# Performance work log

Measured on AMD Instinct MI355X. Metric: run time of the kernel, lower is better.

The kernel has to match this reference:

```python
import jax, jax.numpy as jnp
import numpy as np

K_MASK = -2.3819763e+38
ROPE_THETA = 1000000
MROPE_SECTION = (24, 20, 20)
NORM_EPS = 1e-6


def rms_norm(x, w, eps=NORM_EPS):
    dtype = x.dtype
    x32 = x.astype(jnp.float32)
    rms_inv = jax.lax.rsqrt(jnp.mean(x32 * x32, axis=-1, keepdims=True) + eps)
    return w * (x32 * rms_inv).astype(dtype)


def apply_rope(inputs, positions, head_dim, rope_theta=ROPE_THETA, mrope_section=MROPE_SECTION):
    # positions: [3, B, T] (temporal, height, width); inputs: [B, T, heads, head_dim]
    fraction = 2 * jnp.arange(0, head_dim // 2, dtype=jnp.float32) / head_dim
    timescale = rope_theta ** fraction  # [head_dim//2]
    sinusoid = positions[:, :, :, None].astype(jnp.float32) / timescale  # [3,B,T,hd/2]
    freq = sinusoid[0]
    h_idx = jnp.arange(1, mrope_section[1] * 3, 3)
    w_idx = jnp.arange(2, mrope_section[2] * 3, 3)
    freq = freq.at[..., h_idx].set(sinusoid[1][..., h_idx])
    freq = freq.at[..., w_idx].set(sinusoid[2][..., w_idx])
    freq = freq[:, :, None, :]  # [B,T,1,hd/2]
    sin, cos = jnp.sin(freq), jnp.cos(freq)
    first, second = jnp.split(inputs, 2, axis=-1)
    out = jnp.concatenate([first * cos - second * sin, second * cos + first * sin], axis=-1)
    return out.astype(inputs.dtype)


def setup_inputs() -> dict:
    key = jax.random.key(0)
    ks = jax.random.split(key, 6)
    B, T, D, N, K, H = 2, 1024, 2560, 32, 8, 128
    x = jax.random.normal(ks[0], (B, T, D), dtype=jnp.float32)
    positions = jnp.broadcast_to(jnp.arange(T, dtype=jnp.int32), (3, B, T))
    attn_mask = jnp.tril(jnp.ones((T, T), dtype=bool))[None].repeat(B, axis=0)  # causal [B,T,T]
    wq = jax.random.normal(ks[1], (D, N, H), dtype=jnp.float32) * 0.02
    wk = jax.random.normal(ks[2], (D, K, H), dtype=jnp.float32) * 0.02
    wv = jax.random.normal(ks[3], (D, K, H), dtype=jnp.float32) * 0.02
    wo = jax.random.normal(ks[4], (N, H, D), dtype=jnp.float32) * 0.02
    q_norm_w = jnp.ones((H,), dtype=jnp.float32)
    k_norm_w = jnp.ones((H,), dtype=jnp.float32)
    return {"x": x, "positions": positions, "attn_mask": attn_mask, "wq": wq,
            "wk": wk, "wv": wv, "wo": wo, "q_norm_w": q_norm_w, "k_norm_w": k_norm_w}


def reference(x, positions, attn_mask, wq, wk, wv, wo, q_norm_w, k_norm_w):
    head_dim = wo.shape[1]
    scale = head_dim ** -0.5
    q = rms_norm(jnp.einsum('btd,dnh->btnh', x, wq), q_norm_w)
    k = rms_norm(jnp.einsum('bsd,dkh->bskh', x, wk), k_norm_w)
    v = jnp.einsum('bsd,dkh->bskh', x, wv)
    q = apply_rope(q, positions, head_dim)
    k = apply_rope(k, positions, head_dim)
    b, t, qh, d = q.shape
    _, s, kh, _ = k.shape
    q = q.reshape((b, t, kh, qh // kh, d))  # GQA grouping
    attn = jnp.einsum('bthgd,bshd->bhgts', q, k) * scale
    attn = attn.reshape((b, qh, t, s))
    attn = jnp.where(attn_mask[:, None, :, :], attn, K_MASK)
    attn = jax.nn.softmax(attn.astype(jnp.float32), axis=-1).astype(k.dtype)
    attn = attn.reshape((b, kh, qh // kh, t, s))
    qkv = jnp.einsum('bhgts,bshd->bthgd', attn, v).reshape((b, t, qh, d))
    return jnp.einsum('btnh,nhd->btd', qkv, wo)
```

## Files before the change

kernel.cpp:

```cpp
#include <hip/hip_runtime.h>
#include <hip/hip_bf16.h>

typedef __attribute__((ext_vector_type(8))) __bf16 bf8_t;
typedef __attribute__((ext_vector_type(4))) float f32x4;
typedef __attribute__((ext_vector_type(16))) float f32x16;

#define GLOAD16(gptr, lptr)                                                              \
  __builtin_amdgcn_global_load_lds((const __attribute__((address_space(1))) void*)(gptr), \
                                   (__attribute__((address_space(3))) void*)(lptr), 16, 0, 0)

__device__ __forceinline__ unsigned short f2bf(float f) {
  union { float f; unsigned u; } v; v.f = f;
  return (unsigned short)((v.u + 0x7fffu + ((v.u >> 16) & 1u)) >> 16);
}

__device__ __forceinline__ float bf2f(unsigned short u) {
  union { unsigned u; float f; } v; v.u = ((unsigned)u) << 16;
  return v.f;
}

__device__ __forceinline__ unsigned cvtpk_bf16(float a, float b) {
  unsigned r;
  asm("v_cvt_pk_bf16_f32 %0, %1, %2" : "=v"(r) : "v"(a), "v"(b));
  return r;
}

__global__ void cast_bf16(const float* __restrict__ in, unsigned short* __restrict__ out, int n4) {
  int i = blockIdx.x * blockDim.x + threadIdx.x;
  if (i >= n4) return;
  float4 v = ((const float4*)in)[i];
  ushort4 o;
  o.x = f2bf(v.x); o.y = f2bf(v.y); o.z = f2bf(v.z); o.w = f2bf(v.w);
  ((ushort4*)out)[i] = o;
}

__global__ void tcast(const float* __restrict__ in, unsigned short* __restrict__ out,
                      int R, int C, int ld, int rowOff) {
  __shared__ float tile[32][33];
  int c0 = blockIdx.x * 32, r0 = blockIdx.y * 32;
  int tx = threadIdx.x, ty = threadIdx.y;
#pragma unroll
  for (int i = 0; i < 4; ++i)
    tile[ty + 8 * i][tx] = in[(size_t)(r0 + ty + 8 * i) * C + c0 + tx];
  __syncthreads();
#pragma unroll
  for (int i = 0; i < 4; ++i)
    out[(size_t)(rowOff + c0 + ty + 8 * i) * ld + r0 + tx] = f2bf(tile[tx][ty + 8 * i]);
}

__global__ __launch_bounds__(512, 2) void gemm256(
    const unsigned short* __restrict__ A,
    const unsigned short* __restrict__ Bt,
    float* __restrict__ C0, float* __restrict__ C1,
    unsigned short* __restrict__ Cb,
    int N, int ldk, int Kslice, int nTileN) {
  __shared__ unsigned short SM[4][2][8192];
  int ks = blockIdx.y;
  int kbase = ks * Kslice;
  int nwg = gridDim.x;
  int bidx = blockIdx.x;
  int wg = ((bidx & 7) * (nwg >> 3)) + (bidx >> 3);
  int bm = wg / nTileN, bn = wg % nTileN;
  int m0 = bm << 8, n0 = bn << 8;
  int tid = threadIdx.x, lane = tid & 63, w = tid >> 6;
  int wm = w >> 2, wn = w & 3;
  int lrow = lane & 15, lch = lane >> 4;
  int srow = tid >> 2;
  int scol = ((tid & 3) ^ ((srow >> 1) & 3)) << 3;
  int nt = Kslice >> 5;

  f32x4 acc[8][4] = {};

  auto stage = [&](int t) {
    int buf = t & 3;
    int k0 = kbase + (t << 5);
    const unsigned short* Ag = A + (size_t)(m0 + srow) * ldk + k0 + scol;
    const unsigned short* Bg = Bt + (size_t)(n0 + srow) * ldk + k0 + scol;
    unsigned short* Al = &SM[buf][0][w << 9];
    unsigned short* Bl = &SM[buf][1][w << 9];
    GLOAD16(Ag, Al);
    GLOAD16(Ag + (size_t)128 * ldk, Al + 4096);
    GLOAD16(Bg, Bl);
    GLOAD16(Bg + (size_t)128 * ldk, Bl + 4096);
  };

  stage(0);
  stage(1);
  stage(2);
  for (int t = 0; t < nt; ++t) {
    if (t + 2 < nt)      asm volatile("s_waitcnt vmcnt(8)" ::: "memory");
    else if (t + 1 < nt) asm volatile("s_waitcnt vmcnt(4)" ::: "memory");
    else                 asm volatile("s_waitcnt vmcnt(0)" ::: "memory");
    asm volatile("s_barrier" ::: "memory");
    if (t + 3 < nt) stage(t + 3);
    int buf = t & 3;
    const unsigned short* As = &SM[buf][0][0];
    const unsigned short* Bs = &SM[buf][1][0];
    bf8_t a[8], b[4];
#pragma unroll
    for (int mi = 0; mi < 8; ++mi) {
      int ar = (wm << 7) + (mi << 4) + lrow;
      a[mi] = *(const bf8_t*)(As + ar * 32 + ((lch ^ ((ar >> 1) & 3)) << 3));
    }
#pragma unroll
    for (int ni = 0; ni < 4; ++ni) {
      int br = (wn << 6) + (ni << 4) + lrow;
      b[ni] = *(const bf8_t*)(Bs + br * 32 + ((lch ^ ((br >> 1) & 3)) << 3));
    }
    __builtin_amdgcn_s_setprio(1);
#pragma unroll
    for (int mi = 0; mi < 8; ++mi)
#pragma unroll
      for (int ni = 0; ni < 4; ++ni)
        acc[mi][ni] = __builtin_amdgcn_mfma_f32_16x16x32_bf16(a[mi], b[ni], acc[mi][ni], 0, 0, 0);
    __builtin_amdgcn_s_setprio(0);
  }
  int r0 = m0 + (wm << 7) + (lch << 2);
  int c0 = n0 + (wn << 6) + lrow;
  if (Cb) {
#pragma unroll
    for (int mi = 0; mi < 8; ++mi)
#pragma unroll
      for (int ni = 0; ni < 4; ++ni)
#pragma unroll
        for (int r = 0; r < 4; ++r)
          Cb[(size_t)(r0 + (mi << 4) + r) * N + c0 + (ni << 4)] = f2bf(acc[mi][ni][r]);
  } else {
    float* __restrict__ C = ks ? C1 : C0;
#pragma unroll
    for (int mi = 0; mi < 8; ++mi)
#pragma unroll
      for (int ni = 0; ni < 4; ++ni)
#pragma unroll
        for (int r = 0; r < 4; ++r)
          C[(size_t)(r0 + (mi << 4) + r) * N + c0 + (ni << 4)] = acc[mi][ni][r];
  }
}

__global__ void reduce_add(const float4* __restrict__ a, const float4* __restrict__ b,
                           float4* __restrict__ o, int n4) {
  int i = blockIdx.x * blockDim.x + threadIdx.x;
  if (i >= n4) return;
  float4 x = a[i], y = b[i];
  o[i] = make_float4(x.x + y.x, x.y + y.y, x.z + y.z, x.w + y.w);
}

__global__ __launch_bounds__(128) void normrope(
    const unsigned short* __restrict__ qkv, const int* __restrict__ positions,
    const float* __restrict__ qw, const float* __restrict__ kw,
    unsigned short* __restrict__ qb, unsigned short* __restrict__ kb,
    unsigned short* __restrict__ vt) {
  int blk = blockIdx.x;
  int hh = blk % 48, bt = blk / 48;
  int b = bt >> 10, t = bt & 1023;
  int tid = threadIdx.x;
  int colbase = (hh < 32) ? (hh << 7) : ((hh < 40) ? (4096 + ((hh - 32) << 7)) : (5120 + ((hh - 40) << 7)));
  float val = bf2f(qkv[(size_t)bt * 6144 + colbase + tid]);
  if (hh >= 40) {
    vt[((size_t)((b * 8 + hh - 40) * 128 + tid)) * 1024 + t] = f2bf(val);
    return;
  }
  __shared__ float red[2];
  __shared__ float xs[128];
  float ss = val * val;
#pragma unroll
  for (int m = 32; m >= 1; m >>= 1) ss += __shfl_xor(ss, m);
  if ((tid & 63) == 0) red[tid >> 6] = ss;
  __syncthreads();
  float rinv = rsqrtf((red[0] + red[1]) * (1.0f / 128.0f) + 1e-6f);
  float wgt = (hh < 32) ? qw[tid] : kw[tid];
  float xn = val * rinv * wgt;
  xs[tid] = xn;
  __syncthreads();
  float other = xs[tid ^ 64];
  int pos = positions[b * 1024 + t];
  int j = tid & 63;
  float ang = (float)pos * exp2f(-(float)j * 0.31143075889569027f);
  float sv = sinf(ang), cv = cosf(ang);
  float outv = (tid < 64) ? (xn * cv - other * sv) : (xn * cv + other * sv);
  if (hh >= 32) outv *= 0.12751744f;
  unsigned short o = f2bf(outv);
  if (hh < 32) qb[((size_t)((b * 32 + hh) * 1024 + t)) * 128 + tid] = o;
  else kb[((size_t)((b * 8 + hh - 32) * 1024 + t)) * 128 + tid] = o;
}

__global__ __launch_bounds__(256, 2) void attn(
    const unsigned short* __restrict__ qb,
    const unsigned short* __restrict__ kb,
    const unsigned short* __restrict__ vt,
    unsigned short* __restrict__ ob) {
  __shared__ unsigned short Kl[2][64 * 128];
  __shared__ unsigned short Vl[2][128 * 64];
  int bx = blockIdx.x, hq = blockIdx.y, b = blockIdx.z;
  int qt = (bx < 4) ? (7 - bx) : (bx - 4);
  int kvh = hq >> 2;
  int tid = threadIdx.x, lane = tid & 63, w = tid >> 6;
  int qlane = lane & 31, h = lane >> 5;
  int q0 = (qt << 7) + (w << 5);
  int qg = q0 + qlane;
  const unsigned short* kbase = kb + ((size_t)(b * 8 + kvh) << 17);
  const unsigned short* vbase = vt + ((size_t)(b * 8 + kvh) << 17);

  const unsigned short* qptr = qb + ((size_t)((b * 32 + hq) * 1024 + qg) << 7) + (h << 3);
  bf8_t qf[8];
#pragma unroll
  for (int ds = 0; ds < 8; ++ds) qf[ds] = *(const bf8_t*)(qptr + ds * 16);

  f32x16 o[4] = {};
  float mrun = -3.0e38f, lrun = 0.f;
  int last_st = (q0 + 31) >> 6;
  int nsteps = 2 * qt + 2;

  auto stage = [&](int st, int buf) {
    int s0 = st << 6;
    unsigned short* kd = &Kl[buf][0];
    unsigned short* vd = &Vl[buf][0];
#pragma unroll
    for (int i = 0; i < 4; ++i) {
      int cid = i * 256 + tid;
      int kr = cid >> 4, ksl = cid & 15;
      GLOAD16(kbase + (size_t)(s0 + kr) * 128 + ((ksl ^ (kr & 15)) << 3), kd + cid * 8);
      int vr = cid >> 3, vsl = cid & 7;
      GLOAD16(vbase + (size_t)vr * 1024 + s0 + ((vsl ^ (vr & 7)) << 3), vd + cid * 8);
    }
  };

  stage(0, 0);
  for (int st = 0; st < nsteps; ++st) {
    __syncthreads();
    if (st + 1 < nsteps) stage(st + 1, (st + 1) & 1);
    if (st <= last_st) {
      const char* Kb = (const char*)&Kl[st & 1][0];
      const char* Vb = (const char*)&Vl[st & 1][0];
      f32x16 s0v = {}, s1v = {};
      __builtin_amdgcn_s_setprio(1);
#pragma unroll
      for (int ds = 0; ds < 8; ++ds) {
        int c = ds * 2 + h;
        int r0 = qlane, r1 = 32 + qlane;
        bf8_t k0 = *(const bf8_t*)(Kb + r0 * 256 + ((c ^ (r0 & 15)) << 4));
        bf8_t k1 = *(const bf8_t*)(Kb + r1 * 256 + ((c ^ (r1 & 15)) << 4));
        s0v = __builtin_amdgcn_mfma_f32_32x32x16_bf16(k0, qf[ds], s0v, 0, 0, 0);
        s1v = __builtin_amdgcn_mfma_f32_32x32x16_bf16(k1, qf[ds], s1v, 0, 0, 0);
      }
      __builtin_amdgcn_s_setprio(0);
      bool dm = (st == last_st);
      int kg0 = st << 6;
      float mt = -3.0e38f;
#pragma unroll
      for (int e = 0; e < 16; ++e) {
        int kl = (e & 3) + 8 * (e >> 2) + 4 * h;
        if (dm) {
          if (kg0 + kl > qg) s0v[e] = -3.0e38f;
          if (kg0 + 32 + kl > qg) s1v[e] = -3.0e38f;
        }
        mt = fmaxf(mt, fmaxf(s0v[e], s1v[e]));
      }
      mt = fmaxf(mt, __shfl_xor(mt, 32));
      if (!__all(mt - mrun <= 8.0f)) {
        float mnew = fmaxf(mrun, mt);
        float alpha = exp2f(mrun - mnew);
        lrun *= alpha;
#pragma unroll
        for (int db = 0; db < 4; ++db)
#pragma unroll
          for (int e = 0; e < 16; ++e) o[db][e] *= alpha;
        mrun = mnew;
      }
      float ls = 0.f;
#pragma unroll
      for (int e = 0; e < 16; ++e) {
        s0v[e] = exp2f(s0v[e] - mrun);
        s1v[e] = exp2f(s1v[e] - mrun);
        ls += s0v[e] + s1v[e];
      }
      ls += __shfl_xor(ls, 32);
      lrun += ls;
      bf8_t pf[4];
#pragma unroll
      for (int s = 0; s < 4; ++s) {
        unsigned w00, w01, w10, w11;
        {
          const int B0 = 4 * ((2 * s) & 3);
          if ((2 * s) >> 2) { w00 = cvtpk_bf16(s1v[B0], s1v[B0 + 1]); w01 = cvtpk_bf16(s1v[B0 + 2], s1v[B0 + 3]); }
          else              { w00 = cvtpk_bf16(s0v[B0], s0v[B0 + 1]); w01 = cvtpk_bf16(s0v[B0 + 2], s0v[B0 + 3]); }
        }
        {
          const int B1 = 4 * ((2 * s + 1) & 3);
          if ((2 * s + 1) >> 2) { w10 = cvtpk_bf16(s1v[B1], s1v[B1 + 1]); w11 = cvtpk_bf16(s1v[B1 + 2], s1v[B1 + 3]); }
          else                  { w10 = cvtpk_bf16(s0v[B1], s0v[B1 + 1]); w11 = cvtpk_bf16(s0v[B1 + 2], s0v[B1 + 3]); }
        }
        unsigned sa = h ? w00 : w10, sb = h ? w01 : w11;
        unsigned ra = __shfl_xor(sa, 32), rb = __shfl_xor(sb, 32);
        unsigned ka = h ? w10 : w00, kb2 = h ? w11 : w01;
        unsigned f0 = h ? ra : ka, f1 = h ? rb : kb2;
        unsigned f2 = h ? ka : ra, f3 = h ? kb2 : rb;
        uint4 fv = make_uint4(f0, f1, f2, f3);
        pf[s] = *(bf8_t*)&fv;
      }
      __builtin_amdgcn_s_setprio(1);
#pragma unroll
      for (int db = 0; db < 4; ++db) {
        int vr = (db << 5) + qlane;
#pragma unroll
        for (int s = 0; s < 4; ++s) {
          int c = (s << 1) + h;
          bf8_t vf = *(const bf8_t*)(Vb + vr * 128 + ((c ^ (vr & 7)) << 4));
          o[db] = __builtin_amdgcn_mfma_f32_32x32x16_bf16(vf, pf[s], o[db], 0, 0, 0);
        }
      }
      __builtin_amdgcn_s_setprio(0);
    }
  }

  __syncthreads();
  unsigned short* tb = &Kl[0][0] + (w << 12);
  float inv = 1.0f / lrun;
#pragma unroll
  for (int db = 0; db < 4; ++db)
#pragma unroll
    for (int rq = 0; rq < 4; ++rq) {
      int d0 = (db << 5) + (rq << 3) + (h << 2);
      unsigned lo = ((unsigned)f2bf(o[db][rq * 4 + 1] * inv) << 16) | f2bf(o[db][rq * 4 + 0] * inv);
      unsigned hi = ((unsigned)f2bf(o[db][rq * 4 + 3] * inv) << 16) | f2bf(o[db][rq * 4 + 2] * inv);
      *(uint2*)(tb + qlane * 128 + (d0 ^ ((qlane & 15) << 3))) = make_uint2(lo, hi);
    }
  int rr = lane >> 1, dh = (lane & 1) << 6;
  size_t orow = ((size_t)(b * 1024 + q0 + rr) << 12) + (hq << 7);
#pragma unroll
  for (int i = 0; i < 8; ++i) {
    int d8 = dh + i * 8;
    uint4 vv = *(const uint4*)(tb + rr * 128 + (d8 ^ ((rr & 15) << 3)));
    *(uint4*)(&ob[orow + d8]) = vv;
  }
}

extern "C" void kernel_launch(void* const* d_in, const int* in_sizes, int n_in,
                              void* d_out, int out_size, void* d_ws, size_t ws_size,
                              hipStream_t stream) {
  const float* x = (const float*)d_in[0];
  const int* positions = (const int*)d_in[1];
  const float* wq = (const float*)d_in[3];
  const float* wk = (const float*)d_in[4];
  const float* wv = (const float*)d_in[5];
  const float* wo = (const float*)d_in[6];
  const float* qnw = (const float*)d_in[7];
  const float* knw = (const float*)d_in[8];
  float* out = (float*)d_out;

  char* ws = (char*)d_ws;
  unsigned short* x_bf  = (unsigned short*)(ws);
  unsigned short* wqkvT = (unsigned short*)(ws + 10485760);
  unsigned short* woT   = (unsigned short*)(ws + 41943040);
  unsigned short* qkvb  = (unsigned short*)(ws + 62914560);
  float*          p0    = (float*)(ws + 62914560);
  float*          p1    = (float*)(ws + 83886080);
  unsigned short* q_bf  = (unsigned short*)(ws + 113246208);
  unsigned short* k_bf  = (unsigned short*)(ws + 130023424);
  unsigned short* vt_bf = (unsigned short*)(ws + 134217728);
  unsigned short* a_bf  = (unsigned short*)(ws + 138412032);

  cast_bf16<<<5120, 256, 0, stream>>>(x, x_bf, 2048 * 2560 / 4);
  tcast<<<dim3(128, 80), dim3(32, 8), 0, stream>>>(wq, wqkvT, 2560, 4096, 2560, 0);
  tcast<<<dim3(32, 80), dim3(32, 8), 0, stream>>>(wk, wqkvT, 2560, 1024, 2560, 4096);
  tcast<<<dim3(32, 80), dim3(32, 8), 0, stream>>>(wv, wqkvT, 2560, 1024, 2560, 5120);
  tcast<<<dim3(80, 128), dim3(32, 8), 0, stream>>>(wo, woT, 4096, 2560, 4096, 0);
  gemm256<<<dim3(8 * 24, 1), 512, 0, stream>>>(x_bf, wqkvT, nullptr, nullptr, qkvb,
                                               6144, 2560, 2560, 24);
  normrope<<<2048 * 48, 128, 0, stream>>>(qkvb, positions, qnw, knw, q_bf, k_bf, vt_bf);
  attn<<<dim3(8, 32, 2), 256, 0, stream>>>(q_bf, k_bf, vt_bf, a_bf);
  gemm256<<<dim3(8 * 10, 2), 512, 0, stream>>>(a_bf, woT, p0, p1, nullptr, 2560, 4096, 2048, 10);
  reduce_add<<<5120, 256, 0, stream>>>((const float4*)p0, (const float4*)p1, (float4*)out,
                                       2048 * 2560 / 4);
}
```

Baseline: 282.9 us.

## Vectorize weight transpose-cast, load V directly to registers, three-way split-K output GEMM

Replaces the transpose-cast kernel with a wider variant that reads float4 and writes 16-byte bf16 rows, cutting per-thread memory instructions. The attention kernel no longer stages V through LDS and instead loads V fragments straight from global memory into registers, halving LDS use and async copy traffic. The output projection GEMM moves from a two-way to a three-way split-K with an uneven last slice, and the reduction now sums three partials. This adds more blocks for occupancy but increases partial-buffer traffic, and the direct V loads may expose global latency.

New measurement: 288.9 us. +2.1%, slower.

```diff
diff --git a/kernel.cpp b/kernel.cpp
--- a/kernel.cpp
+++ b/kernel.cpp
@@ -34,29 +34,48 @@
   ((ushort4*)out)[i] = o;
 }
 
-__global__ void tcast(const float* __restrict__ in, unsigned short* __restrict__ out,
-                      int R, int C, int ld, int rowOff) {
-  __shared__ float tile[32][33];
-  int c0 = blockIdx.x * 32, r0 = blockIdx.y * 32;
-  int tx = threadIdx.x, ty = threadIdx.y;
+__global__ __launch_bounds__(256) void tcast4(const float* __restrict__ in,
+                                              unsigned short* __restrict__ out,
+                                              int C, int ld, int rowOff) {
+  __shared__ float tile[128][40];
+  int c0 = blockIdx.x * 128, r0 = blockIdx.y * 32;
+  int tid = threadIdx.x;
+  int tx = tid & 31, ty = tid >> 5;
+  float4 v[4];
 #pragma unroll
   for (int i = 0; i < 4; ++i)
-    tile[ty + 8 * i][tx] = in[(size_t)(r0 + ty + 8 * i) * C + c0 + tx];
+    v[i] = *(const float4*)(in + (size_t)(r0 + (ty << 2) + i) * C + c0 + (tx << 2));
+#pragma unroll
+  for (int j = 0; j < 4; ++j) {
+    float4 t4 = make_float4(v[0].x, v[1].x, v[2].x, v[3].x);
+    if (j == 1) t4 = make_float4(v[0].y, v[1].y, v[2].y, v[3].y);
+    if (j == 2) t4 = make_float4(v[0].z, v[1].z, v[2].z, v[3].z);
+    if (j == 3) t4 = make_float4(v[0].w, v[1].w, v[2].w, v[3].w);
+    *(float4*)(&tile[(tx << 2) + j][ty << 2]) = t4;
+  }
   __syncthreads();
-#pragma unroll
-  for (int i = 0; i < 4; ++i)
-    out[(size_t)(rowOff + c0 + ty + 8 * i) * ld + r0 + tx] = f2bf(tile[tx][ty + 8 * i]);
+  int p = tid & 3;
+#pragma unroll
+  for (int half = 0; half < 2; ++half) {
+    int cc = (tid >> 2) + half * 64;
+    const float* row = &tile[cc][p << 3];
+    unsigned u0 = ((unsigned)f2bf(row[1]) << 16) | f2bf(row[0]);
+    unsigned u1 = ((unsigned)f2bf(row[3]) << 16) | f2bf(row[2]);
+    unsigned u2 = ((unsigned)f2bf(row[5]) << 16) | f2bf(row[4]);
+    unsigned u3 = ((unsigned)f2bf(row[7]) << 16) | f2bf(row[6]);
+    *(uint4*)(out + (size_t)(rowOff + c0 + cc) * ld + r0 + (p << 3)) = make_uint4(u0, u1, u2, u3);
+  }
 }
 
 __global__ __launch_bounds__(512, 2) void gemm256(
     const unsigned short* __restrict__ A,
     const unsigned short* __restrict__ Bt,
-    float* __restrict__ C0, float* __restrict__ C1,
-    unsigned short* __restrict__ Cb,
-    int N, int ldk, int Kslice, int nTileN) {
+    float* __restrict__ Cf, unsigned short* __restrict__ Cb,
+    int N, int ldk, int Ks0, int Ktot, int nTileN, long long pstride) {
   __shared__ unsigned short SM[4][2][8192];
   int ks = blockIdx.y;
-  int kbase = ks * Kslice;
+  int kbase = ks * Ks0;
+  int Kslice = (ks == (int)gridDim.y - 1) ? (Ktot - kbase) : Ks0;
   int nwg = gridDim.x;
   int bidx = blockIdx.x;
   int wg = ((bidx & 7) * (nwg >> 3)) + (bidx >> 3);
@@ -126,7 +145,7 @@
         for (int r = 0; r < 4; ++r)
           Cb[(size_t)(r0 + (mi << 4) + r) * N + c0 + (ni << 4)] = f2bf(acc[mi][ni][r]);
   } else {
-    float* __restrict__ C = ks ? C1 : C0;
+    float* __restrict__ C = Cf + (size_t)ks * pstride;
 #pragma unroll
     for (int mi = 0; mi < 8; ++mi)
 #pragma unroll
@@ -137,12 +156,12 @@
   }
 }
 
-__global__ void reduce_add(const float4* __restrict__ a, const float4* __restrict__ b,
-                           float4* __restrict__ o, int n4) {
+__global__ void reduce3(const float4* __restrict__ a, const float4* __restrict__ b,
+                        const float4* __restrict__ c, float4* __restrict__ o, int n4) {
   int i = blockIdx.x * blockDim.x + threadIdx.x;
   if (i >= n4) return;
-  float4 x = a[i], y = b[i];
-  o[i] = make_float4(x.x + y.x, x.y + y.y, x.z + y.z, x.w + y.w);
+  float4 x = a[i], y = b[i], z = c[i];
+  o[i] = make_float4(x.x + y.x + z.x, x.y + y.y + z.y, x.z + y.z + z.z, x.w + y.w + z.w);
 }
 
 __global__ __launch_bounds__(128) void normrope(
@@ -190,7 +209,6 @@
     const unsigned short* __restrict__ vt,
     unsigned short* __restrict__ ob) {
   __shared__ unsigned short Kl[2][64 * 128];
-  __shared__ unsigned short Vl[2][128 * 64];
   int bx = blockIdx.x, hq = blockIdx.y, b = blockIdx.z;
   int qt = (bx < 4) ? (7 - bx) : (bx - 4);
   int kvh = hq >> 2;
@@ -214,14 +232,11 @@
   auto stage = [&](int st, int buf) {
     int s0 = st << 6;
     unsigned short* kd = &Kl[buf][0];
-    unsigned short* vd = &Vl[buf][0];
 #pragma unroll
     for (int i = 0; i < 4; ++i) {
       int cid = i * 256 + tid;
       int kr = cid >> 4, ksl = cid & 15;
       GLOAD16(kbase + (size_t)(s0 + kr) * 128 + ((ksl ^ (kr & 15)) << 3), kd + cid * 8);
-      int vr = cid >> 3, vsl = cid & 7;
-      GLOAD16(vbase + (size_t)vr * 1024 + s0 + ((vsl ^ (vr & 7)) << 3), vd + cid * 8);
     }
   };
 
@@ -231,7 +246,7 @@
     if (st + 1 < nsteps) stage(st + 1, (st + 1) & 1);
     if (st <= last_st) {
       const char* Kb = (const char*)&Kl[st & 1][0];
-      const char* Vb = (const char*)&Vl[st & 1][0];
+      int s0 = st << 6;
       f32x16 s0v = {}, s1v = {};
       __builtin_amdgcn_s_setprio(1);
 #pragma unroll
@@ -244,15 +259,22 @@
         s1v = __builtin_amdgcn_mfma_f32_32x32x16_bf16(k1, qf[ds], s1v, 0, 0, 0);
       }
       __builtin_amdgcn_s_setprio(0);
+      bf8_t vf[4][4];
+#pragma unroll
+      for (int db = 0; db < 4; ++db) {
+        const unsigned short* vr = vbase + (size_t)((db << 5) + qlane) * 1024 + s0;
+#pragma unroll
+        for (int s = 0; s < 4; ++s)
+          vf[db][s] = *(const bf8_t*)(vr + ((s << 1) + h) * 8);
+      }
       bool dm = (st == last_st);
-      int kg0 = st << 6;
       float mt = -3.0e38f;
 #pragma unroll
       for (int e = 0; e < 16; ++e) {
         int kl = (e & 3) + 8 * (e >> 2) + 4 * h;
         if (dm) {
-          if (kg0 + kl > qg) s0v[e] = -3.0e38f;
-          if (kg0 + 32 + kl > qg) s1v[e] = -3.0e38f;
+          if (s0 + kl > qg) s0v[e] = -3.0e38f;
+          if (s0 + 32 + kl > qg) s1v[e] = -3.0e38f;
         }
         mt = fmaxf(mt, fmaxf(s0v[e], s1v[e]));
       }
@@ -300,15 +322,10 @@
       }
       __builtin_amdgcn_s_setprio(1);
 #pragma unroll
-      for (int db = 0; db < 4; ++db) {
-        int vr = (db << 5) + qlane;
-#pragma unroll
-        for (int s = 0; s < 4; ++s) {
-          int c = (s << 1) + h;
-          bf8_t vf = *(const bf8_t*)(Vb + vr * 128 + ((c ^ (vr & 7)) << 4));
-          o[db] = __builtin_amdgcn_mfma_f32_32x32x16_bf16(vf, pf[s], o[db], 0, 0, 0);
-        }
-      }
+      for (int db = 0; db < 4; ++db)
+#pragma unroll
+        for (int s = 0; s < 4; ++s)
+          o[db] = __builtin_amdgcn_mfma_f32_32x32x16_bf16(vf[db][s], pf[s], o[db], 0, 0, 0);
       __builtin_amdgcn_s_setprio(0);
     }
   }
@@ -354,22 +371,24 @@
   unsigned short* woT   = (unsigned short*)(ws + 41943040);
   unsigned short* qkvb  = (unsigned short*)(ws + 62914560);
   float*          p0    = (float*)(ws + 62914560);
-  float*          p1    = (float*)(ws + 83886080);
   unsigned short* q_bf  = (unsigned short*)(ws + 113246208);
   unsigned short* k_bf  = (unsigned short*)(ws + 130023424);
   unsigned short* vt_bf = (unsigned short*)(ws + 134217728);
   unsigned short* a_bf  = (unsigned short*)(ws + 138412032);
+  const long long PSTR = 2048LL * 2560;
 
   cast_bf16<<<5120, 256, 0, stream>>>(x, x_bf, 2048 * 2560 / 4);
-  tcast<<<dim3(128, 80), dim3(32, 8), 0, stream>>>(wq, wqkvT, 2560, 4096, 2560, 0);
-  tcast<<<dim3(32, 80), dim3(32, 8), 0, stream>>>(wk, wqkvT, 2560, 1024, 2560, 4096);
-  tcast<<<dim3(32, 80), dim3(32, 8), 0, stream>>>(wv, wqkvT, 2560, 1024, 2560, 5120);
-  tcast<<<dim3(80, 128), dim3(32, 8), 0, stream>>>(wo, woT, 4096, 2560, 4096, 0);
-  gemm256<<<dim3(8 * 24, 1), 512, 0, stream>>>(x_bf, wqkvT, nullptr, nullptr, qkvb,
-                                               6144, 2560, 2560, 24);
+  tcast4<<<dim3(32, 80), 256, 0, stream>>>(wq, wqkvT, 4096, 2560, 0);
+  tcast4<<<dim3(8, 80), 256, 0, stream>>>(wk, wqkvT, 1024, 2560, 4096);
+  tcast4<<<dim3(8, 80), 256, 0, stream>>>(wv, wqkvT, 1024, 2560, 5120);
+  tcast4<<<dim3(20, 128), 256, 0, stream>>>(wo, woT, 2560, 4096, 0);
+  gemm256<<<dim3(192, 1), 512, 0, stream>>>(x_bf, wqkvT, nullptr, qkvb,
+                                            6144, 2560, 2560, 2560, 24, 0);
   normrope<<<2048 * 48, 128, 0, stream>>>(qkvb, positions, qnw, knw, q_bf, k_bf, vt_bf);
   attn<<<dim3(8, 32, 2), 256, 0, stream>>>(q_bf, k_bf, vt_bf, a_bf);
-  gemm256<<<dim3(8 * 10, 2), 512, 0, stream>>>(a_bf, woT, p0, p1, nullptr, 2560, 4096, 2048, 10);
-  reduce_add<<<5120, 256, 0, stream>>>((const float4*)p0, (const float4*)p1, (float4*)out,
-                                       2048 * 2560 / 4);
-}
+  gemm256<<<dim3(80, 3), 512, 0, stream>>>(a_bf, woT, p0, nullptr,
+                                           2560, 4096, 1344, 4096, 10, PSTR);
+  reduce3<<<5120, 256, 0, stream>>>((const float4*)p0, (const float4*)(p0 + PSTR),
+                                    (const float4*)(p0 + 2 * PSTR), (float4*)out,
+                                    2048 * 2560 / 4);
+}
```
